# Kernel optimization log

Hardware: AMD Instinct MI355X
Metric: run time of the kernel (lower is better)

Reference implementation:

```python
import jax, jax.numpy as jnp
import numpy as np

NODELEN = 394
N_NODES = 50000
N_EDGES = 200000
IN_DIM = 2 * NODELEN  # 788
H2 = 192
EMB = 128


def setup_inputs() -> dict:
    key = jax.random.key(0)
    ks = jax.random.split(key, 12)
    inp = {
        'features': jax.random.normal(ks[0], (N_NODES, NODELEN), dtype=jnp.float32),
        'src': jax.random.randint(ks[1], (N_EDGES,), 0, N_NODES),
        'dst': jax.random.randint(ks[2], (N_EDGES,), 0, N_NODES),
        # AutoEncoder params (Linear weights stored as [in, out])
        'W_enc1': jax.random.normal(ks[3], (IN_DIM, H2), dtype=jnp.float32) / np.sqrt(IN_DIM),
        'b_enc1': jnp.zeros((H2,), dtype=jnp.float32),
        'W_enc3': jax.random.normal(ks[4], (H2, EMB), dtype=jnp.float32) / np.sqrt(H2),
        'b_enc3': jnp.zeros((EMB,), dtype=jnp.float32),
        'W_dec1': jax.random.normal(ks[5], (EMB, H2), dtype=jnp.float32) / np.sqrt(EMB),
        'b_dec1': jnp.zeros((H2,), dtype=jnp.float32),
        'W_dec3': jax.random.normal(ks[6], (H2, IN_DIM), dtype=jnp.float32) / np.sqrt(H2),
        'b_dec3': jnp.zeros((IN_DIM,), dtype=jnp.float32),
    }
    return inp


def _segment_mean(msgs, dst, inv_deg, n):
    # msgs: [E, F] gathered neighbor features; mean over incoming edges per node
    return jax.ops.segment_sum(msgs, dst, num_segments=n) * inv_deg


def reference(features, src, dst, W_enc1, b_enc1, W_enc3, b_enc3,
              W_dec1, b_dec1, W_dec3, b_dec3):
    n = features.shape[0]
    ones = jnp.ones(src.shape[0], dtype=features.dtype)
    deg = jax.ops.segment_sum(ones, dst, num_segments=n)
    # nodes with no neighbors fall back to the zero dummy vector (as in source)
    inv_deg = (1.0 / jnp.maximum(deg, 1.0))[:, None]

    # depth-1 aggregation: mean of raw neighbor features, then feat[0] := 0
    h1 = _segment_mean(features[src], dst, inv_deg, n)
    h1 = h1.at[:, 0].set(0.0)
    # depth-2 aggregation: mean of depth-1 aggregates of neighbors, feat[0] := 0
    h2 = _segment_mean(h1[src], dst, inv_deg, n)
    h2 = h2.at[:, 0].set(0.0)

    # concatenated embedding with positions 0 and NODELEN zeroed
    emb = jnp.concatenate([features, h2], axis=1)  # [N, 788]
    emb = emb.at[:, 0].set(0.0).at[:, NODELEN].set(0.0)

    # AutoEncoder forward (dropout is identity at inference)
    x = jax.nn.relu(emb @ W_enc1 + b_enc1)
    encoded = x @ W_enc3 + b_enc3
    y = jax.nn.relu(encoded @ W_dec1 + b_dec1)
    decoded = y @ W_dec3 + b_dec3
    return encoded, decoded, emb
```

## Files before the change

### kernel.cpp

```cpp
#include <hip/hip_runtime.h>
#include <hip/hip_bf16.h>

#define NODELEN 394
#define IN_DIM 788
#define H2DIM 192
#define EMBDIM 128
#define NCHUNK 197

typedef __attribute__((ext_vector_type(4))) float f32x4;
typedef __attribute__((ext_vector_type(8))) short bfrag;

static __device__ __forceinline__ unsigned short f2bf(float f) {
    union { float f; unsigned u; } v; v.f = f;
    unsigned r = v.u + 0x7FFFu + ((v.u >> 16) & 1u);
    return (unsigned short)(r >> 16);
}
static __device__ __forceinline__ float bf2f(unsigned short h) {
    union { unsigned u; float f; } v; v.u = ((unsigned)h) << 16;
    return v.f;
}


__global__ void count_deg(const int* __restrict__ dst, int* __restrict__ deg, int e) {
    int i = blockIdx.x * blockDim.x + threadIdx.x;
    if (i < e) atomicAdd(&deg[dst[i]], 1);
}

__global__ void block_sum(const int* __restrict__ deg, int* __restrict__ bsum, int n) {
    __shared__ int s[256];
    int t = threadIdx.x;
    int i = blockIdx.x * 256 + t;
    s[t] = (i < n) ? deg[i] : 0;
    __syncthreads();
    for (int d = 128; d > 0; d >>= 1) {
        if (t < d) s[t] += s[t + d];
        __syncthreads();
    }
    if (t == 0) bsum[blockIdx.x] = s[0];
}

__global__ void scan_bsums(int* bsum, int nb) {
    __shared__ int s[256];
    int t = threadIdx.x;
    int x0 = (t < nb) ? bsum[t] : 0;
    s[t] = x0;
    __syncthreads();
    for (int d = 1; d < 256; d <<= 1) {
        int u = (t >= d) ? s[t - d] : 0;
        __syncthreads();
        s[t] += u;
        __syncthreads();
    }
    if (t < nb) bsum[t] = s[t] - x0;
}

__global__ void block_scan(const int* __restrict__ deg, const int* __restrict__ boff,
                           int* __restrict__ rowstart, int* __restrict__ cursor, int n) {
    __shared__ int s[256];
    int t = threadIdx.x;
    int i = blockIdx.x * 256 + t;
    int x0 = (i < n) ? deg[i] : 0;
    s[t] = x0;
    __syncthreads();
    for (int d = 1; d < 256; d <<= 1) {
        int u = (t >= d) ? s[t - d] : 0;
        __syncthreads();
        s[t] += u;
        __syncthreads();
    }
    if (i < n) {
        int r = boff[blockIdx.x] + s[t] - x0;
        rowstart[i] = r;
        cursor[i] = r;
    }
}

__global__ void inv_deg_k(const int* __restrict__ deg, float* __restrict__ inv, int n) {
    int i = blockIdx.x * blockDim.x + threadIdx.x;
    if (i < n) inv[i] = 1.0f / fmaxf((float)deg[i], 1.0f);
}

__global__ void fill_edges(const int* __restrict__ src, const int* __restrict__ dst,
                           int* __restrict__ cursor, int* __restrict__ elist, int e) {
    int i = blockIdx.x * blockDim.x + threadIdx.x;
    if (i < e) {
        int p = atomicAdd(&cursor[dst[i]], 1);
        elist[p] = src[i];
    }
}


__global__ __launch_bounds__(256) void gather1(
        const float* __restrict__ feat, const int* __restrict__ rowstart,
        const int* __restrict__ deg, const float* __restrict__ inv,
        const int* __restrict__ elist, unsigned short* __restrict__ h1) {
    const int node = blockIdx.x;
    const int c = threadIdx.x;
    if (c >= NCHUNK) return;
    const int beg = rowstart[node];
    const int dc = deg[node];
    const float s = inv[node];
    const size_t off = (size_t)c * 2;

    float ax = 0.f, ay = 0.f, bx = 0.f, by = 0.f;
    float cx = 0.f, cy = 0.f, dx = 0.f, dy = 0.f;
    int j = 0;
    for (; j + 3 < dc; j += 4) {
        int n0 = elist[beg + j], n1 = elist[beg + j + 1];
        int n2 = elist[beg + j + 2], n3 = elist[beg + j + 3];
        float2 v0 = *(const float2*)(feat + (size_t)n0 * NODELEN + off);
        float2 v1 = *(const float2*)(feat + (size_t)n1 * NODELEN + off);
        float2 v2 = *(const float2*)(feat + (size_t)n2 * NODELEN + off);
        float2 v3 = *(const float2*)(feat + (size_t)n3 * NODELEN + off);
        ax += v0.x; ay += v0.y; bx += v1.x; by += v1.y;
        cx += v2.x; cy += v2.y; dx += v3.x; dy += v3.y;
    }
    for (; j < dc; ++j) {
        int n0 = elist[beg + j];
        float2 v0 = *(const float2*)(feat + (size_t)n0 * NODELEN + off);
        ax += v0.x; ay += v0.y;
    }
    float fx = (ax + bx + cx + dx) * s;
    float fy = (ay + by + cy + dy) * s;
    if (c == 0) fx = 0.f;
    unsigned out = ((unsigned)f2bf(fy) << 16) | (unsigned)f2bf(fx);
    *(unsigned*)(h1 + (size_t)node * NODELEN + off) = out;
}

__global__ __launch_bounds__(256) void gather2_emb(
        const float* __restrict__ feat, const unsigned* __restrict__ h1,
        const int* __restrict__ rowstart, const int* __restrict__ deg,
        const float* __restrict__ inv, const int* __restrict__ elist,
        float* __restrict__ emb) {
    const int node = blockIdx.x;
    const int c = threadIdx.x;
    if (c >= NCHUNK) return;
    const int beg = rowstart[node];
    const int dc = deg[node];
    const float s = inv[node];
    const size_t h1row2 = (size_t)NODELEN / 2;

    float ax = 0.f, ay = 0.f, bx = 0.f, by = 0.f;
    float cx = 0.f, cy = 0.f, dx = 0.f, dy = 0.f;
    int j = 0;
    for (; j + 3 < dc; j += 4) {
        int n0 = elist[beg + j], n1 = elist[beg + j + 1];
        int n2 = elist[beg + j + 2], n3 = elist[beg + j + 3];
        unsigned u0 = h1[(size_t)n0 * NCHUNK + c];
        unsigned u1 = h1[(size_t)n1 * NCHUNK + c];
        unsigned u2 = h1[(size_t)n2 * NCHUNK + c];
        unsigned u3 = h1[(size_t)n3 * NCHUNK + c];
        ax += bf2f((unsigned short)u0); ay += bf2f((unsigned short)(u0 >> 16));
        bx += bf2f((unsigned short)u1); by += bf2f((unsigned short)(u1 >> 16));
        cx += bf2f((unsigned short)u2); cy += bf2f((unsigned short)(u2 >> 16));
        dx += bf2f((unsigned short)u3); dy += bf2f((unsigned short)(u3 >> 16));
    }
    for (; j < dc; ++j) {
        int n0 = elist[beg + j];
        unsigned u0 = h1[(size_t)n0 * NCHUNK + c];
        ax += bf2f((unsigned short)u0); ay += bf2f((unsigned short)(u0 >> 16));
    }
    float hx = (ax + bx + cx + dx) * s;
    float hy = (ay + by + cy + dy) * s;

    const float* fr = feat + (size_t)node * NODELEN;
    float* er = emb + (size_t)node * IN_DIM;
    float2 fv = *(const float2*)(fr + c * 2);
    if (c == 0) { fv.x = 0.f; hx = 0.f; }
    *(float2*)(er + c * 2) = fv;
    float2 hv; hv.x = hx; hv.y = hy;
    *(float2*)(er + NODELEN + c * 2) = hv;
}

__global__ void transpose_w(const float* __restrict__ W, unsigned short* __restrict__ Wt,
                            int K, int N, int Kp) {
    int idx = blockIdx.x * 256 + threadIdx.x;
    if (idx >= N * Kp) return;
    int nrow = idx / Kp, k = idx - nrow * Kp;
    Wt[idx] = (k < K) ? f2bf(W[(size_t)k * N + nrow]) : (unsigned short)0;
}

template <int MF, int NF, int RELU, int A_F32, int OUTF, int OUTB>
__global__ __launch_bounds__(256) void gemm_mfma(
    const void* __restrict__ Aptr, const unsigned short* __restrict__ Wt,
    const float* __restrict__ bias, float* __restrict__ Cf,
    unsigned short* __restrict__ Cb, int M, int N, int K, int Ksteps)
{
    constexpr int BMr = 32 * MF;
    constexpr int BNr = 32 * NF;
    __shared__ unsigned short As[BMr][40];
    __shared__ unsigned short Bs[BNr][40];

    const int tid = threadIdx.x;
    const int wid = tid >> 6, l = tid & 63;
    const int wm = wid >> 1, wn = wid & 1;
    const int lr = l & 15, lk = l >> 4;
    const int m0 = blockIdx.x * BMr;
    const int n0 = blockIdx.y * BNr;
    const int Kp = Ksteps * 32;

    f32x4 acc[MF][NF];
    #pragma unroll
    for (int i = 0; i < MF; ++i)
        #pragma unroll
        for (int j = 0; j < NF; ++j)
            acc[i][j] = (f32x4){0.f, 0.f, 0.f, 0.f};

    float bv[NF];
    #pragma unroll
    for (int j = 0; j < NF; ++j) {
        int gn = n0 + wn * NF * 16 + j * 16 + lr;
        bv[j] = (gn < N) ? bias[gn] : 0.f;
    }

    for (int kt = 0; kt < Ksteps; ++kt) {
        int k0 = kt * 32;
        if (A_F32) {
            const float* A = (const float*)Aptr;
            for (int a = tid; a < BMr * 4; a += 256) {
                int row = a >> 2, q = a & 3;
                int gm = m0 + row, gk = k0 + q * 8;
                float4 v0 = make_float4(0.f, 0.f, 0.f, 0.f);
                float4 v1 = make_float4(0.f, 0.f, 0.f, 0.f);
                if (gm < M) {
                    if (gk < K)     v0 = *(const float4*)(A + (size_t)gm * K + gk);
                    if (gk + 4 < K) v1 = *(const float4*)(A + (size_t)gm * K + gk + 4);
                }
                union { unsigned short u[8]; bfrag v; } pk;
                pk.u[0] = f2bf(v0.x); pk.u[1] = f2bf(v0.y);
                pk.u[2] = f2bf(v0.z); pk.u[3] = f2bf(v0.w);
                pk.u[4] = f2bf(v1.x); pk.u[5] = f2bf(v1.y);
                pk.u[6] = f2bf(v1.z); pk.u[7] = f2bf(v1.w);
                *(bfrag*)&As[row][q * 8] = pk.v;
            }
        } else {
            const unsigned short* A = (const unsigned short*)Aptr;
            for (int a = tid; a < BMr * 2; a += 256) {
                int row = a >> 1, h = a & 1;
                int gm = m0 + row;
                bfrag v0 = {0,0,0,0,0,0,0,0}, v1 = {0,0,0,0,0,0,0,0};
                if (gm < M) {
                    const unsigned short* p = A + (size_t)gm * K + k0 + h * 16;
                    v0 = *(const bfrag*)p;
                    v1 = *(const bfrag*)(p + 8);
                }
                *(bfrag*)&As[row][h * 16]     = v0;
                *(bfrag*)&As[row][h * 16 + 8] = v1;
            }
        }
        for (int a = tid; a < BNr * 2; a += 256) {
            int row = a >> 1, h = a & 1;
            int gn = n0 + row;
            bfrag v0 = {0,0,0,0,0,0,0,0}, v1 = {0,0,0,0,0,0,0,0};
            if (gn < N) {
                const unsigned short* p = Wt + (size_t)gn * Kp + k0 + h * 16;
                v0 = *(const bfrag*)p;
                v1 = *(const bfrag*)(p + 8);
            }
            *(bfrag*)&Bs[row][h * 16]     = v0;
            *(bfrag*)&Bs[row][h * 16 + 8] = v1;
        }
        __syncthreads();

        bfrag af[MF], bfr[NF];
        #pragma unroll
        for (int i = 0; i < MF; ++i)
            af[i] = *(const bfrag*)&As[wm * MF * 16 + i * 16 + lr][lk * 8];
        #pragma unroll
        for (int j = 0; j < NF; ++j)
            bfr[j] = *(const bfrag*)&Bs[wn * NF * 16 + j * 16 + lr][lk * 8];
        #pragma unroll
        for (int i = 0; i < MF; ++i)
            #pragma unroll
            for (int j = 0; j < NF; ++j)
                acc[i][j] = __builtin_amdgcn_mfma_f32_16x16x32_bf16(af[i], bfr[j], acc[i][j], 0, 0, 0);
        __syncthreads();
    }

    #pragma unroll
    for (int i = 0; i < MF; ++i) {
        #pragma unroll
        for (int j = 0; j < NF; ++j) {
            #pragma unroll
            for (int r = 0; r < 4; ++r) {
                int gm = m0 + wm * MF * 16 + i * 16 + lk * 4 + r;
                int gn = n0 + wn * NF * 16 + j * 16 + lr;
                if (gm < M && gn < N) {
                    float v = acc[i][j][r] + bv[j];
                    if (RELU) v = fmaxf(v, 0.f);
                    if (OUTF) Cf[(size_t)gm * N + gn] = v;
                    if (OUTB) Cb[(size_t)gm * N + gn] = f2bf(v);
                }
            }
        }
    }
}


extern "C" void kernel_launch(void* const* d_in, const int* in_sizes, int n_in,
                              void* d_out, int out_size, void* d_ws, size_t ws_size,
                              hipStream_t stream) {
    const float* features = (const float*)d_in[0];
    const int*   src      = (const int*)d_in[1];
    const int*   dst      = (const int*)d_in[2];
    const float* W_enc1   = (const float*)d_in[3];
    const float* b_enc1   = (const float*)d_in[4];
    const float* W_enc3   = (const float*)d_in[5];
    const float* b_enc3   = (const float*)d_in[6];
    const float* W_dec1   = (const float*)d_in[7];
    const float* b_dec1   = (const float*)d_in[8];
    const float* W_dec3   = (const float*)d_in[9];
    const float* b_dec3   = (const float*)d_in[10];

    const int n = in_sizes[0] / NODELEN;
    const int e = in_sizes[1];

    float* encoded = (float*)d_out;
    float* decoded = encoded + (size_t)n * EMBDIM;
    float* emb     = decoded + (size_t)n * IN_DIM;

    char* ws = (char*)d_ws;
    unsigned short* h1    = (unsigned short*)(ws + 0);
    unsigned short* x16   = (unsigned short*)(ws + 0);
    unsigned short* enc16 = (unsigned short*)(ws + 19200000);
    unsigned short* y16   = (unsigned short*)(ws + 32000000);
    unsigned short* Wt1   = (unsigned short*)(ws + 52000000);
    unsigned short* Wt2   = (unsigned short*)(ws + 52400000);
    unsigned short* Wt3   = (unsigned short*)(ws + 52500000);
    unsigned short* Wt4   = (unsigned short*)(ws + 52600000);
    float* inv            = (float*)(ws + 53000000);
    int*   deg            = (int*)  (ws + 53200000);
    int*   rowstart       = (int*)  (ws + 53400000);
    int*   cursor         = (int*)  (ws + 53600000);
    int*   elist          = (int*)  (ws + 53800000);
    int*   bsum           = (int*)  (ws + 54600000);

    const int nb = (n + 255) / 256;
    const int eb = (e + 255) / 256;

    transpose_w<<<(192 * 800 + 255) / 256, 256, 0, stream>>>(W_enc1, Wt1, IN_DIM, H2DIM, 800);
    transpose_w<<<(128 * 192 + 255) / 256, 256, 0, stream>>>(W_enc3, Wt2, H2DIM, EMBDIM, 192);
    transpose_w<<<(192 * 128 + 255) / 256, 256, 0, stream>>>(W_dec1, Wt3, EMBDIM, H2DIM, 128);
    transpose_w<<<(788 * 192 + 255) / 256, 256, 0, stream>>>(W_dec3, Wt4, H2DIM, IN_DIM, 192);

    hipMemsetAsync(deg, 0, (size_t)n * sizeof(int), stream);
    count_deg<<<eb, 256, 0, stream>>>(dst, deg, e);
    block_sum<<<nb, 256, 0, stream>>>(deg, bsum, n);
    scan_bsums<<<1, 256, 0, stream>>>(bsum, nb);
    block_scan<<<nb, 256, 0, stream>>>(deg, bsum, rowstart, cursor, n);
    inv_deg_k<<<nb, 256, 0, stream>>>(deg, inv, n);
    fill_edges<<<eb, 256, 0, stream>>>(src, dst, cursor, elist, e);

    gather1<<<n, 256, 0, stream>>>(features, rowstart, deg, inv, elist, h1);
    gather2_emb<<<n, 256, 0, stream>>>(features, (const unsigned*)h1, rowstart, deg, inv, elist, emb);

    gemm_mfma<2, 6, 1, 1, 0, 1><<<dim3(782, 1), 256, 0, stream>>>(
        emb, Wt1, b_enc1, nullptr, x16, n, H2DIM, IN_DIM, 25);
    gemm_mfma<4, 4, 0, 0, 1, 1><<<dim3(391, 1), 256, 0, stream>>>(
        x16, Wt2, b_enc3, encoded, enc16, n, EMBDIM, H2DIM, 6);
    gemm_mfma<2, 6, 1, 0, 0, 1><<<dim3(782, 1), 256, 0, stream>>>(
        enc16, Wt3, b_dec1, nullptr, y16, n, H2DIM, EMBDIM, 4);
    gemm_mfma<4, 4, 0, 0, 1, 0><<<dim3(391, 7), 256, 0, stream>>>(
        y16, Wt4, b_dec3, decoded, nullptr, n, IN_DIM, H2DIM, 6);
}
```

Before: 388.0 us.

## Emit bf16 embedding copy from gather, fuse small kernels, retile GEMMs

The second gather kernel now also writes a padded bf16 copy of the embedding when workspace allows, so the first encoder GEMM reads bf16 instead of re-reading and converting the fp32 embedding. Four weight-transpose launches are merged into one, and the inverse-degree computation is folded into the scan kernel. GEMM tiles are enlarged (MF=4, and NF=6 for the last GEMM), cutting grid size. This relies on a larger workspace and adds extra write traffic for the bf16 copy.

```diff
diff --git a/kernel.cpp b/kernel.cpp
--- a/kernel.cpp
+++ b/kernel.cpp
@@ -55,7 +55,8 @@
 }
 
 __global__ void block_scan(const int* __restrict__ deg, const int* __restrict__ boff,
-                           int* __restrict__ rowstart, int* __restrict__ cursor, int n) {
+                           int* __restrict__ rowstart, int* __restrict__ cursor,
+                           float* __restrict__ inv, int n) {
     __shared__ int s[256];
     int t = threadIdx.x;
     int i = blockIdx.x * 256 + t;
@@ -72,12 +73,8 @@
         int r = boff[blockIdx.x] + s[t] - x0;
         rowstart[i] = r;
         cursor[i] = r;
-    }
-}
-
-__global__ void inv_deg_k(const int* __restrict__ deg, float* __restrict__ inv, int n) {
-    int i = blockIdx.x * blockDim.x + threadIdx.x;
-    if (i < n) inv[i] = 1.0f / fmaxf((float)deg[i], 1.0f);
+        inv[i] = 1.0f / fmaxf((float)x0, 1.0f);
+    }
 }
 
 __global__ void fill_edges(const int* __restrict__ src, const int* __restrict__ dst,
@@ -131,14 +128,20 @@
         const float* __restrict__ feat, const unsigned* __restrict__ h1,
         const int* __restrict__ rowstart, const int* __restrict__ deg,
         const float* __restrict__ inv, const int* __restrict__ elist,
-        float* __restrict__ emb) {
+        float* __restrict__ emb, unsigned* __restrict__ emb16) {
     const int node = blockIdx.x;
     const int c = threadIdx.x;
-    if (c >= NCHUNK) return;
+    if (c >= NCHUNK) {
+        if (emb16 && c >= NCHUNK && c < NCHUNK + 3) {
+            int p = 394 + (c - NCHUNK) * 2;
+            emb16[(size_t)node * 400 + p] = 0u;
+            emb16[(size_t)node * 400 + p + 1] = 0u;
+        }
+        return;
+    }
     const int beg = rowstart[node];
     const int dc = deg[node];
     const float s = inv[node];
-    const size_t h1row2 = (size_t)NODELEN / 2;
 
     float ax = 0.f, ay = 0.f, bx = 0.f, by = 0.f;
     float cx = 0.f, cy = 0.f, dx = 0.f, dy = 0.f;
@@ -170,21 +173,44 @@
     *(float2*)(er + c * 2) = fv;
     float2 hv; hv.x = hx; hv.y = hy;
     *(float2*)(er + NODELEN + c * 2) = hv;
-}
-
-__global__ void transpose_w(const float* __restrict__ W, unsigned short* __restrict__ Wt,
-                            int K, int N, int Kp) {
-    int idx = blockIdx.x * 256 + threadIdx.x;
-    if (idx >= N * Kp) return;
+
+    if (emb16) {
+        unsigned* e16 = emb16 + (size_t)node * 400;
+        e16[c]          = ((unsigned)f2bf(fv.y) << 16) | (unsigned)f2bf(fv.x);
+        e16[NCHUNK + c] = ((unsigned)f2bf(hy)  << 16) | (unsigned)f2bf(hx);
+    }
+}
+
+__device__ __forceinline__ void tr_one(const float* W, unsigned short* Wt,
+                                       int K, int N, int Kp, int idx) {
     int nrow = idx / Kp, k = idx - nrow * Kp;
     Wt[idx] = (k < K) ? f2bf(W[(size_t)k * N + nrow]) : (unsigned short)0;
+}
+
+#define T1E (192 * 800)
+#define T2E (128 * 192)
+#define T3E (192 * 128)
+#define T4E (788 * 192)
+
+__global__ void transpose_all(const float* __restrict__ W1, unsigned short* __restrict__ Wt1,
+                              const float* __restrict__ W2, unsigned short* __restrict__ Wt2,
+                              const float* __restrict__ W3, unsigned short* __restrict__ Wt3,
+                              const float* __restrict__ W4, unsigned short* __restrict__ Wt4) {
+    int idx = blockIdx.x * 256 + threadIdx.x;
+    if (idx < T1E) { tr_one(W1, Wt1, IN_DIM, H2DIM, 800, idx); return; }
+    idx -= T1E;
+    if (idx < T2E) { tr_one(W2, Wt2, H2DIM, EMBDIM, 192, idx); return; }
+    idx -= T2E;
+    if (idx < T3E) { tr_one(W3, Wt3, EMBDIM, H2DIM, 128, idx); return; }
+    idx -= T3E;
+    if (idx < T4E) { tr_one(W4, Wt4, H2DIM, IN_DIM, 192, idx); return; }
 }
 
 template <int MF, int NF, int RELU, int A_F32, int OUTF, int OUTB>
 __global__ __launch_bounds__(256) void gemm_mfma(
     const void* __restrict__ Aptr, const unsigned short* __restrict__ Wt,
     const float* __restrict__ bias, float* __restrict__ Cf,
-    unsigned short* __restrict__ Cb, int M, int N, int K, int Ksteps)
+    unsigned short* __restrict__ Cb, int M, int N, int K, int lda, int Ksteps)
 {
     constexpr int BMr = 32 * MF;
     constexpr int BNr = 32 * NF;
@@ -223,8 +249,8 @@
                 float4 v0 = make_float4(0.f, 0.f, 0.f, 0.f);
                 float4 v1 = make_float4(0.f, 0.f, 0.f, 0.f);
                 if (gm < M) {
-                    if (gk < K)     v0 = *(const float4*)(A + (size_t)gm * K + gk);
-                    if (gk + 4 < K) v1 = *(const float4*)(A + (size_t)gm * K + gk + 4);
+                    if (gk < K)     v0 = *(const float4*)(A + (size_t)gm * lda + gk);
+                    if (gk + 4 < K) v1 = *(const float4*)(A + (size_t)gm * lda + gk + 4);
                 }
                 union { unsigned short u[8]; bfrag v; } pk;
                 pk.u[0] = f2bf(v0.x); pk.u[1] = f2bf(v0.y);
@@ -240,7 +266,7 @@
                 int gm = m0 + row;
                 bfrag v0 = {0,0,0,0,0,0,0,0}, v1 = {0,0,0,0,0,0,0,0};
                 if (gm < M) {
-                    const unsigned short* p = A + (size_t)gm * K + k0 + h * 16;
+                    const unsigned short* p = A + (size_t)gm * lda + k0 + h * 16;
                     v0 = *(const bfrag*)p;
                     v1 = *(const bfrag*)(p + 8);
                 }
@@ -320,46 +346,78 @@
     float* emb     = decoded + (size_t)n * IN_DIM;
 
     char* ws = (char*)d_ws;
-    unsigned short* h1    = (unsigned short*)(ws + 0);
-    unsigned short* x16   = (unsigned short*)(ws + 0);
-    unsigned short* enc16 = (unsigned short*)(ws + 19200000);
-    unsigned short* y16   = (unsigned short*)(ws + 32000000);
-    unsigned short* Wt1   = (unsigned short*)(ws + 52000000);
-    unsigned short* Wt2   = (unsigned short*)(ws + 52400000);
-    unsigned short* Wt3   = (unsigned short*)(ws + 52500000);
-    unsigned short* Wt4   = (unsigned short*)(ws + 52600000);
-    float* inv            = (float*)(ws + 53000000);
-    int*   deg            = (int*)  (ws + 53200000);
-    int*   rowstart       = (int*)  (ws + 53400000);
-    int*   cursor         = (int*)  (ws + 53600000);
-    int*   elist          = (int*)  (ws + 53800000);
-    int*   bsum           = (int*)  (ws + 54600000);
+    const size_t NEED_A = 134000000;
+    const int useA = (ws_size >= NEED_A) ? 1 : 0;
+
+    unsigned short* emb16;
+    unsigned short* h1;
+    unsigned short* x16, *enc16, *y16;
+    unsigned short* Wt1, *Wt2, *Wt3, *Wt4;
+    float* inv; int *deg, *rowstart, *cursor, *elist, *bsum;
+
+    if (useA) {
+        emb16    = (unsigned short*)(ws + 0);
+        h1       = (unsigned short*)(ws + 80000000);
+        x16      = (unsigned short*)(ws + 80000000);
+        enc16    = (unsigned short*)(ws + 99200000);
+        y16      = (unsigned short*)(ws + 112000000);
+        Wt1      = (unsigned short*)(ws + 131200000);
+        Wt2      = (unsigned short*)(ws + 131600000);
+        Wt3      = (unsigned short*)(ws + 131700000);
+        Wt4      = (unsigned short*)(ws + 131800000);
+        inv      = (float*)(ws + 132200000);
+        deg      = (int*)  (ws + 132400000);
+        rowstart = (int*)  (ws + 132600000);
+        cursor   = (int*)  (ws + 132800000);
+        elist    = (int*)  (ws + 133000000);
+        bsum     = (int*)  (ws + 133800000);
+    } else {
+        emb16    = nullptr;
+        h1       = (unsigned short*)(ws + 0);
+        x16      = (unsigned short*)(ws + 0);
+        enc16    = (unsigned short*)(ws + 19200000);
+        y16      = (unsigned short*)(ws + 32000000);
+        Wt1      = (unsigned short*)(ws + 52000000);
+        Wt2      = (unsigned short*)(ws + 52400000);
+        Wt3      = (unsigned short*)(ws + 52500000);
+        Wt4      = (unsigned short*)(ws + 52600000);
+        inv      = (float*)(ws + 53000000);
+        deg      = (int*)  (ws + 53200000);
+        rowstart = (int*)  (ws + 53400000);
+        cursor   = (int*)  (ws + 53600000);
+        elist    = (int*)  (ws + 53800000);
+        bsum     = (int*)  (ws + 54600000);
+    }
 
     const int nb = (n + 255) / 256;
     const int eb = (e + 255) / 256;
 
-    transpose_w<<<(192 * 800 + 255) / 256, 256, 0, stream>>>(W_enc1, Wt1, IN_DIM, H2DIM, 800);
-    transpose_w<<<(128 * 192 + 255) / 256, 256, 0, stream>>>(W_enc3, Wt2, H2DIM, EMBDIM, 192);
-    transpose_w<<<(192 * 128 + 255) / 256, 256, 0, stream>>>(W_dec1, Wt3, EMBDIM, H2DIM, 128);
-    transpose_w<<<(788 * 192 + 255) / 256, 256, 0, stream>>>(W_dec3, Wt4, H2DIM, IN_DIM, 192);
+    transpose_all<<<(T1E + T2E + T3E + T4E + 255) / 256, 256, 0, stream>>>(
+        W_enc1, Wt1, W_enc3, Wt2, W_dec1, Wt3, W_dec3, Wt4);
 
     hipMemsetAsync(deg, 0, (size_t)n * sizeof(int), stream);
     count_deg<<<eb, 256, 0, stream>>>(dst, deg, e);
     block_sum<<<nb, 256, 0, stream>>>(deg, bsum, n);
     scan_bsums<<<1, 256, 0, stream>>>(bsum, nb);
-    block_scan<<<nb, 256, 0, stream>>>(deg, bsum, rowstart, cursor, n);
-    inv_deg_k<<<nb, 256, 0, stream>>>(deg, inv, n);
+    block_scan<<<nb, 256, 0, stream>>>(deg, bsum, rowstart, cursor, inv, n);
     fill_edges<<<eb, 256, 0, stream>>>(src, dst, cursor, elist, e);
 
     gather1<<<n, 256, 0, stream>>>(features, rowstart, deg, inv, elist, h1);
-    gather2_emb<<<n, 256, 0, stream>>>(features, (const unsigned*)h1, rowstart, deg, inv, elist, emb);
-
-    gemm_mfma<2, 6, 1, 1, 0, 1><<<dim3(782, 1), 256, 0, stream>>>(
-        emb, Wt1, b_enc1, nullptr, x16, n, H2DIM, IN_DIM, 25);
-    gemm_mfma<4, 4, 0, 0, 1, 1><<<dim3(391, 1), 256, 0, stream>>>(
-        x16, Wt2, b_enc3, encoded, enc16, n, EMBDIM, H2DIM, 6);
-    gemm_mfma<2, 6, 1, 0, 0, 1><<<dim3(782, 1), 256, 0, stream>>>(
-        enc16, Wt3, b_dec1, nullptr, y16, n, H2DIM, EMBDIM, 4);
-    gemm_mfma<4, 4, 0, 0, 1, 0><<<dim3(391, 7), 256, 0, stream>>>(
-        y16, Wt4, b_dec3, decoded, nullptr, n, IN_DIM, H2DIM, 6);
-}
+    gather2_emb<<<n, 256, 0, stream>>>(features, (const unsigned*)h1, rowstart, deg,
+                                       inv, elist, emb, (unsigned*)emb16);
+
+    const int MB = (n + 127) / 128;
+    if (useA) {
+        gemm_mfma<4, 6, 1, 0, 0, 1><<<dim3(MB, 1), 256, 0, stream>>>(
+            emb16, Wt1, b_enc1, nullptr, x16, n, H2DIM, 800, 800, 25);
+    } else {
+        gemm_mfma<4, 6, 1, 1, 0, 1><<<dim3(MB, 1), 256, 0, stream>>>(
+            emb, Wt1, b_enc1, nullptr, x16, n, H2DIM, IN_DIM, IN_DIM, 25);
+    }
+    gemm_mfma<4, 4, 0, 0, 1, 1><<<dim3(MB, 1), 256, 0, stream>>>(
+        x16, Wt2, b_enc3, encoded, enc16, n, EMBDIM, H2DIM, H2DIM, 6);
+    gemm_mfma<4, 6, 1, 0, 0, 1><<<dim3(MB, 1), 256, 0, stream>>>(
+        enc16, Wt3, b_dec1, nullptr, y16, n, H2DIM, EMBDIM, EMBDIM, 4);
+    gemm_mfma<4, 6, 0, 0, 1, 0><<<dim3(MB, 5), 256, 0, stream>>>(
+        y16, Wt4, b_dec3, decoded, nullptr, n, IN_DIM, H2DIM, H2DIM, 6);
+}
```

After: 420.7 us. 1.08x slower.
